# Optimization experiments

Measured on AMD Instinct MI355X. Metric: run time of the kernel, lower is better.

The kernel has to match this reference:

```python
import jax, jax.numpy as jnp
import numpy as np

T = 200                      # TRAIN_ROIS_PER_IMAGE
RATIO = 0.33                 # ROI_POSITIVE_RATIO
P_MAX = int(T * RATIO)       # max positive ROIs (66)
MH, MW = 28, 28              # MASK_SHAPE
STD = jnp.array([0.1, 0.1, 0.2, 0.2], jnp.float32)  # BBOX_STD_DEV
EPS = 1e-6


def _iou(a, b):
    # a [N,4], b [G,4] -> [N,G] IoU (same math as overlaps_graph, without tiling)
    ay1, ax1, ay2, ax2 = a[:, 0:1], a[:, 1:2], a[:, 2:3], a[:, 3:4]
    by1, bx1, by2, bx2 = b[None, :, 0], b[None, :, 1], b[None, :, 2], b[None, :, 3]
    iy = jnp.maximum(jnp.minimum(ay2, by2) - jnp.maximum(ay1, by1), 0.0)
    ix = jnp.maximum(jnp.minimum(ax2, bx2) - jnp.maximum(ax1, bx1), 0.0)
    inter = iy * ix
    union = (ay2 - ay1) * (ax2 - ax1) + (by2 - by1) * (bx2 - bx1) - inter
    return inter / jnp.maximum(union, EPS)


def _box_refinement(box, gt):
    # standard Mask R-CNN box_refinement_graph
    h = jnp.maximum(box[:, 2] - box[:, 0], EPS)
    w = jnp.maximum(box[:, 3] - box[:, 1], EPS)
    cy = box[:, 0] + 0.5 * h
    cx = box[:, 1] + 0.5 * w
    gh = jnp.maximum(gt[:, 2] - gt[:, 0], EPS)
    gw = jnp.maximum(gt[:, 3] - gt[:, 1], EPS)
    gcy = gt[:, 0] + 0.5 * gh
    gcx = gt[:, 1] + 0.5 * gw
    return jnp.stack([(gcy - cy) / h, (gcx - cx) / w,
                      jnp.log(gh / h), jnp.log(gw / w)], axis=-1)


def _crop_and_resize(imgs, boxes):
    # imgs [T,H,W], boxes [T,4] normalized; TF crop_and_resize bilinear semantics,
    # extrapolation_value = 0 for samples outside [0, H-1] x [0, W-1].
    Tn, H, W = imgs.shape
    y1, x1, y2, x2 = boxes[:, 0], boxes[:, 1], boxes[:, 2], boxes[:, 3]
    iy = jnp.arange(MH, dtype=jnp.float32)
    ix = jnp.arange(MW, dtype=jnp.float32)
    ys = y1[:, None] * (H - 1) + iy[None, :] * ((y2 - y1) * (H - 1) / (MH - 1))[:, None]  # [T,MH]
    xs = x1[:, None] * (W - 1) + ix[None, :] * ((x2 - x1) * (W - 1) / (MW - 1))[:, None]  # [T,MW]
    y0 = jnp.floor(ys); x0 = jnp.floor(xs)
    wy = (ys - y0)[:, :, None]
    wx = (xs - x0)[:, None, :]
    y0i = jnp.clip(y0, 0, H - 1).astype(jnp.int32)
    y1i = jnp.clip(y0 + 1, 0, H - 1).astype(jnp.int32)
    x0i = jnp.clip(x0, 0, W - 1).astype(jnp.int32)
    x1i = jnp.clip(x0 + 1, 0, W - 1).astype(jnp.int32)
    t = jnp.arange(Tn)[:, None, None]
    v00 = imgs[t, y0i[:, :, None], x0i[:, None, :]]
    v01 = imgs[t, y0i[:, :, None], x1i[:, None, :]]
    v10 = imgs[t, y1i[:, :, None], x0i[:, None, :]]
    v11 = imgs[t, y1i[:, :, None], x1i[:, None, :]]
    val = (v00 * (1 - wx) + v01 * wx) * (1 - wy) + (v10 * (1 - wx) + v11 * wx) * wy
    ok = ((ys >= 0) & (ys <= H - 1))[:, :, None] & ((xs >= 0) & (xs <= W - 1))[:, None, :]
    return jnp.where(ok, val, 0.0)


def _targets_one(proposals, class_ids, boxes, masks):
    # proposals [N,4], class_ids [G] int, boxes [G,4], masks [H,W,G]
    N = proposals.shape[0]
    # zero-padding trim expressed as validity masks (jit-friendly fixed shapes)
    valid_prop = jnp.any(proposals != 0, axis=1)
    valid_gt = jnp.any(boxes != 0, axis=1)
    non_crowd = (class_ids > 0) & valid_gt
    crowd = (class_ids < 0) & valid_gt

    ov = _iou(proposals, boxes)                              # [N,G]
    ov_nc = jnp.where(non_crowd[None, :], ov, -1.0)          # mask crowd/padded gt
    roi_iou_max = ov_nc.max(axis=1)
    crowd_max = jnp.where(crowd[None, :], ov, 0.0).max(axis=1)

    pos_mask = valid_prop & (roi_iou_max >= 0.5)
    neg_mask = valid_prop & (roi_iou_max < 0.5) & (crowd_max < 0.001)

    # deterministic selection (original uses tf.random.shuffle): positives first-in-order
    pos_order = jnp.argsort(jnp.where(pos_mask, 0, 1))
    neg_order = jnp.argsort(jnp.where(neg_mask, 0, 1))
    pos_count = jnp.minimum(pos_mask.sum(), P_MAX)
    neg_needed = jnp.floor(pos_count.astype(jnp.float32) / RATIO).astype(jnp.int32) - pos_count
    neg_count = jnp.minimum(jnp.minimum(neg_needed, neg_mask.sum()), T - pos_count)

    slot = jnp.arange(T)
    is_pos = slot < pos_count
    is_neg = (slot >= pos_count) & (slot < pos_count + neg_count)
    src = jnp.where(is_pos,
                    pos_order[jnp.clip(slot, 0, N - 1)],
                    neg_order[jnp.clip(slot - pos_count, 0, N - 1)])
    rois = jnp.where((is_pos | is_neg)[:, None], proposals[src], 0.0)

    assign = jnp.argmax(ov_nc[src], axis=1)                  # gt assignment per slot
    gt_box = boxes[assign]
    gt_cls = jnp.where(is_pos, class_ids[assign], 0)

    deltas = _box_refinement(rois, gt_box) / STD
    deltas = jnp.where(is_pos[:, None], deltas, 0.0)

    # USE_MINI_MASK: roi box in gt-box-normalized coordinates
    gy1, gx1, gy2, gx2 = gt_box[:, 0], gt_box[:, 1], gt_box[:, 2], gt_box[:, 3]
    gh = jnp.maximum(gy2 - gy1, EPS)
    gw = jnp.maximum(gx2 - gx1, EPS)
    mm = jnp.stack([(rois[:, 0] - gy1) / gh, (rois[:, 1] - gx1) / gw,
                    (rois[:, 2] - gy1) / gh, (rois[:, 3] - gx1) / gw], axis=-1)

    roi_masks = jnp.moveaxis(jnp.take(masks, assign, axis=2), 2, 0)  # [T,H,W]
    m = jnp.round(_crop_and_resize(roi_masks, mm))
    m = jnp.where(is_pos[:, None, None], m, 0.0)
    return rois, gt_cls, deltas, m


def setup_inputs() -> dict:
    key = jax.random.key(0)
    ks = jax.random.split(key, 4)
    B, N, G, HM = 16, 2000, 200, 56

    def boxes_of(k, shape):
        k1, k2, k3, k4 = jax.random.split(k, 4)
        y1 = jax.random.uniform(k1, shape) * 0.5
        x1 = jax.random.uniform(k2, shape) * 0.5
        h = 0.1 + jax.random.uniform(k3, shape) * 0.4
        w = 0.1 + jax.random.uniform(k4, shape) * 0.4
        return jnp.stack([y1, x1, y1 + h, x1 + w], axis=-1)

    proposals = boxes_of(ks[0], (B, N))
    proposals = proposals * (jnp.arange(N) < N - 200)[None, :, None]  # zero-padded tail
    prior_class_ids = jax.random.randint(ks[1], (B, G), -1, 81).astype(jnp.int32)  # -1=crowd, 0=padding
    prior_boxes = boxes_of(ks[2], (B, G)) * (prior_class_ids != 0)[..., None]
    prior_masks = (jax.random.uniform(ks[3], (B, HM, HM, G)) > 0.5).astype(jnp.float32)
    return {"proposals": proposals, "prior_class_ids": prior_class_ids,
            "prior_boxes": prior_boxes, "prior_masks": prior_masks}


def reference(proposals, prior_class_ids, prior_boxes, prior_masks):
    rois, cls, deltas, masks = jax.vmap(_targets_one)(proposals, prior_class_ids,
                                                      prior_boxes, prior_masks)
    return rois, cls, deltas, masks
```

## Files before the change

kernel.cpp:

```cpp
#include <hip/hip_runtime.h>
#include <math.h>

#pragma clang fp contract(off)

#define BN    16
#define NP    2000
#define NG    200
#define NT    200
#define PMAX  66
#define EPSF  1e-6f
#define MH    28
#define MW    28
#define HM    56
#define NPIX  (HM*HM)
#define NW    49
#define NGP   256

#define KA_BLOCKS 128
#define KG_BLOCKS (49*4*BN)

__global__ __launch_bounds__(256) void kF(
    const float* __restrict__ proposals, const int* __restrict__ cls_ids,
    const float* __restrict__ boxes, const float* __restrict__ masks,
    int* __restrict__ flag_ws, int* __restrict__ assign_ws,
    unsigned long long* __restrict__ bits)
{
#pragma clang fp contract(off)
  const int tid  = threadIdx.x;
  const int lane = tid & 63;
  const int wv   = tid >> 6;

  __shared__ float4 gbox[NG];
  __shared__ float  garea[NG];
  __shared__ int    gflag[NG];
  __shared__ unsigned long long sw[64];

  if (blockIdx.x < KA_BLOCKS) {
    const int b = blockIdx.x >> 3;
    const int bxa = blockIdx.x & 7;

    for (int j = tid; j < NG; j += 256) {
      float4 g = reinterpret_cast<const float4*>(boxes + (size_t)b * NG * 4)[j];
      int c = cls_ids[b * NG + j];
      bool vg = (g.x != 0.f) || (g.y != 0.f) || (g.z != 0.f) || (g.w != 0.f);
      gbox[j]  = g;
      garea[j] = (g.z - g.x) * (g.w - g.y);
      gflag[j] = vg ? (c > 0 ? 1 : (c < 0 ? 2 : 0)) : 0;
    }
    __syncthreads();

    int i = bxa * 256 + tid;
    if (i >= NP) return;

    float4 p = reinterpret_cast<const float4*>(proposals + (size_t)b * NP * 4)[i];
    bool vp = (p.x != 0.f) || (p.y != 0.f) || (p.z != 0.f) || (p.w != 0.f);
    float pa = (p.z - p.x) * (p.w - p.y);

    float best = -3.0e38f;
    int   bestj = 0;
    float cmax = 0.f;
    for (int j = 0; j < NG; ++j) {
      float4 g = gbox[j];
      float iy = fmaxf(fminf(p.z, g.z) - fmaxf(p.x, g.x), 0.f);
      float ix = fmaxf(fminf(p.w, g.w) - fmaxf(p.y, g.y), 0.f);
      float inter = iy * ix;
      float uni = (pa + garea[j]) - inter;
      float iou = inter / fmaxf(uni, EPSF);
      int fl = gflag[j];
      float v = (fl == 1) ? iou : -1.0f;
      if (v > best) { best = v; bestj = j; }
      if (fl == 2) cmax = fmaxf(cmax, iou);
    }
    bool pos = vp && (best >= 0.5f);
    bool neg = vp && (best < 0.5f) && (cmax < 0.001f);
    flag_ws[b * NP + i]   = pos ? 1 : (neg ? 2 : 0);
    assign_ws[b * NP + i] = bestj;
  } else {
    int idx = blockIdx.x - KA_BLOCKS;
    const int pword = idx % 49;
    idx /= 49;
    const int gw0 = (idx & 3) * 64;
    const int b   = idx >> 2;
    const int p0  = pword * 64;

    const bool gok = (gw0 + lane) < NG;
    const float* mbase = masks + (size_t)b * NPIX * NG + gw0 + lane;
    for (int e = 0; e < 16; ++e) {
      int pl = e * 4 + wv;
      float v = 0.f;
      if (gok) v = mbase[(size_t)(p0 + pl) * NG];
      unsigned long long word = __ballot(v != 0.f);
      if (lane == 0) sw[pl] = word;
    }
    __syncthreads();

    unsigned long long w0 = sw[lane];
    for (int k = 0; k < 16; ++k) {
      int gl = wv * 16 + k;
      unsigned long long word = __ballot((int)((w0 >> gl) & 1ULL));
      if (lane == 0 && (gw0 + gl) < NG)
        bits[(size_t)(b * NGP + gw0 + gl) * NW + pword] = word;
    }
  }
}

__global__ __launch_bounds__(256) void kB(
    const float* __restrict__ proposals, const int* __restrict__ cls_ids,
    const float* __restrict__ boxes, const int* __restrict__ flag_ws,
    const int* __restrict__ assign_ws, float* __restrict__ out,
    float* __restrict__ mm_ws, int* __restrict__ ma_ws)
{
#pragma clang fp contract(off)
  const int b = blockIdx.x;
  const int tid = threadIdx.x;
  const int lane = tid & 63;
  const int wv = tid >> 6;

  __shared__ unsigned short pos_list[NP];
  __shared__ unsigned short neg_list[NP];
  __shared__ int wcp[4], wcn[4];
  __shared__ int s_pt, s_nt;
  if (tid == 0) { s_pt = 0; s_nt = 0; }
  __syncthreads();

  const int* fb = flag_ws + b * NP;
  for (int base = 0; base < NP; base += 256) {
    int i = base + tid;
    int f = (i < NP) ? fb[i] : 0;
    bool isp = (f == 1), isn = (f == 2);
    unsigned long long bp = __ballot(isp);
    unsigned long long bn = __ballot(isn);
    __syncthreads();
    if (lane == 0) { wcp[wv] = __popcll(bp); wcn[wv] = __popcll(bn); }
    __syncthreads();
    int prep = __popcll(bp & ((1ull << lane) - 1ull));
    int pren = __popcll(bn & ((1ull << lane) - 1ull));
    int bpp = 0, bnn = 0, tp = 0, tn = 0;
    for (int w = 0; w < 4; ++w) {
      if (w < wv) { bpp += wcp[w]; bnn += wcn[w]; }
      tp += wcp[w]; tn += wcn[w];
    }
    int pt = s_pt, nt = s_nt;
    if (isp) pos_list[pt + bpp + prep] = (unsigned short)i;
    if (isn) neg_list[nt + bnn + pren] = (unsigned short)i;
    __syncthreads();
    if (tid == 0) { s_pt = pt + tp; s_nt = nt + tn; }
  }
  __syncthreads();

  int pos_total = s_pt, neg_total = s_nt;
  int pos_count = min(pos_total, PMAX);
  int neg_needed = (int)floorf((float)pos_count / 0.33f) - pos_count;
  int neg_count = min(min(neg_needed, neg_total), NT - pos_count);

  if (tid < NT) {
    bool ispos = tid < pos_count;
    bool isneg = (!ispos) && (tid < pos_count + neg_count);
    float r0 = 0.f, r1 = 0.f, r2 = 0.f, r3 = 0.f;
    float d0 = 0.f, d1 = 0.f, d2 = 0.f, d3 = 0.f;
    float m0 = 0.f, m1 = 0.f, m2 = 0.f, m3 = 0.f;
    float clsf = 0.f;
    int ma = -1;
    if (ispos || isneg) {
      int i = ispos ? (int)pos_list[tid] : (int)neg_list[tid - pos_count];
      float4 p = reinterpret_cast<const float4*>(proposals + (size_t)b * NP * 4)[i];
      r0 = p.x; r1 = p.y; r2 = p.z; r3 = p.w;
      if (ispos) {
        int a = assign_ws[b * NP + i];
        ma = a;
        float4 g = reinterpret_cast<const float4*>(boxes + (size_t)b * NG * 4)[a];
        float h  = fmaxf(r2 - r0, EPSF);
        float w  = fmaxf(r3 - r1, EPSF);
        float cy = r0 + 0.5f * h;
        float cx = r1 + 0.5f * w;
        float gh = fmaxf(g.z - g.x, EPSF);
        float gw = fmaxf(g.w - g.y, EPSF);
        float gcy = g.x + 0.5f * gh;
        float gcx = g.y + 0.5f * gw;
        d0 = ((gcy - cy) / h) / 0.1f;
        d1 = ((gcx - cx) / w) / 0.1f;
        d2 = logf(gh / h) / 0.2f;
        d3 = logf(gw / w) / 0.2f;
        m0 = (r0 - g.x) / gh;
        m1 = (r1 - g.y) / gw;
        m2 = (r2 - g.x) / gh;
        m3 = (r3 - g.y) / gw;
        clsf = (float)cls_ids[b * NG + a];
      }
    }
    int s = b * NT + tid;
    float* rois = out;
    float* cls  = out + BN * NT * 4;
    float* dlt  = out + BN * NT * 4 + BN * NT;
    rois[s * 4 + 0] = r0; rois[s * 4 + 1] = r1;
    rois[s * 4 + 2] = r2; rois[s * 4 + 3] = r3;
    cls[s] = clsf;
    dlt[s * 4 + 0] = d0; dlt[s * 4 + 1] = d1;
    dlt[s * 4 + 2] = d2; dlt[s * 4 + 3] = d3;
    mm_ws[s * 4 + 0] = m0; mm_ws[s * 4 + 1] = m1;
    mm_ws[s * 4 + 2] = m2; mm_ws[s * 4 + 3] = m3;
    ma_ws[s] = ma;
  }
}

__global__ __launch_bounds__(256) void kC(
    const unsigned long long* __restrict__ bits, const float* __restrict__ mm_ws,
    const int* __restrict__ ma_ws, float* __restrict__ out)
{
#pragma clang fp contract(off)
  const int s = blockIdx.x;
  float4* om = reinterpret_cast<float4*>(
      out + (size_t)(BN * NT * 9) + (size_t)s * (MH * MW));
  const int q = threadIdx.x;
  const int a = ma_ws[s];
  if (a < 0) {
    if (q < (MH * MW) / 4) om[q] = make_float4(0.f, 0.f, 0.f, 0.f);
    return;
  }

  __shared__ unsigned long long pb[NW];
  const int b = s / NT;
  if (q < NW) pb[q] = bits[(size_t)(b * NGP + a) * NW + q];
  __syncthreads();
  if (q >= (MH * MW) / 4) return;

  float y1 = mm_ws[s * 4 + 0], x1 = mm_ws[s * 4 + 1];
  float y2 = mm_ws[s * 4 + 2], x2 = mm_ws[s * 4 + 3];
  float sy = (y2 - y1) * 55.0f / 27.0f;
  float sx = (x2 - x1) * 55.0f / 27.0f;

  int px0 = q * 4;
  int my  = px0 / MW;
  float ys = y1 * 55.0f + (float)my * sy;
  float y0f = floorf(ys);
  float wy  = ys - y0f;
  int y0i = (int)fminf(fmaxf(y0f, 0.f), 55.f);
  int y1i = (int)fminf(fmaxf(y0f + 1.0f, 0.f), 55.f);
  bool oky = (ys >= 0.f) && (ys <= 55.f);
  const int r0b = y0i * HM;
  const int r1b = y1i * HM;

  float res[4];
  for (int k = 0; k < 4; ++k) {
    int mx = (px0 + k) - my * MW;
    float xs = x1 * 55.0f + (float)mx * sx;
    float x0f = floorf(xs);
    float wx  = xs - x0f;
    int x0i = (int)fminf(fmaxf(x0f, 0.f), 55.f);
    int x1i = (int)fminf(fmaxf(x0f + 1.0f, 0.f), 55.f);
    int p00 = r0b + x0i, p01 = r0b + x1i;
    int p10 = r1b + x0i, p11 = r1b + x1i;
    float v00 = (float)((pb[p00 >> 6] >> (p00 & 63)) & 1ULL);
    float v01 = (float)((pb[p01 >> 6] >> (p01 & 63)) & 1ULL);
    float v10 = (float)((pb[p10 >> 6] >> (p10 & 63)) & 1ULL);
    float v11 = (float)((pb[p11 >> 6] >> (p11 & 63)) & 1ULL);
    float val = (v00 * (1.f - wx) + v01 * wx) * (1.f - wy)
              + (v10 * (1.f - wx) + v11 * wx) * wy;
    bool ok = oky && (xs >= 0.f) && (xs <= 55.f);
    res[k] = ok ? rintf(val) : 0.f;
  }
  om[q] = make_float4(res[0], res[1], res[2], res[3]);
}

extern "C" void kernel_launch(void* const* d_in, const int* in_sizes, int n_in,
                              void* d_out, int out_size, void* d_ws, size_t ws_size,
                              hipStream_t stream)
{
  const float* proposals = (const float*)d_in[0];
  const int*   cls_ids   = (const int*)d_in[1];
  const float* boxes     = (const float*)d_in[2];
  const float* masks     = (const float*)d_in[3];
  float* out = (float*)d_out;

  char* ws = (char*)d_ws;
  int*   flag_ws   = (int*)ws;    ws += (size_t)BN * NP * sizeof(int);
  int*   assign_ws = (int*)ws;    ws += (size_t)BN * NP * sizeof(int);
  float* mm_ws     = (float*)ws;  ws += (size_t)BN * NT * 4 * sizeof(float);
  int*   ma_ws     = (int*)ws;    ws += (size_t)BN * NT * sizeof(int);
  unsigned long long* bits_ws = (unsigned long long*)ws;

  kF<<<KA_BLOCKS + KG_BLOCKS, 256, 0, stream>>>(
      proposals, cls_ids, boxes, masks, flag_ws, assign_ws, bits_ws);
  kB<<<BN, 256, 0, stream>>>(proposals, cls_ids, boxes, flag_ws, assign_ws,
                             out, mm_ws, ma_ws);
  kC<<<BN * NT, 256, 0, stream>>>(bits_ws, mm_ws, ma_ws, out);
}
```

Measured before the change: 112.3 us.

## Fuse ROI selection and mask crop into one kernel via ballot bitmasks

The IoU stage now writes per-wave ballot bitmasks of positive and negative proposals instead of per-proposal flags. The separate compaction kernel and mask kernel are merged into a single kernel with one block per output ROI. Each block popcounts the bitmasks to get the counts and finds its proposal with a rank-select scan, then crops the mask directly. This removes one kernel launch, the serial per-image compaction loop, and the intermediate mm/ma workspace round trip. The cost is that every block redundantly recomputes the counts and does a bit-clearing select loop that can run for up to about 64 iterations.

```diff
diff --git a/kernel.cpp b/kernel.cpp
--- a/kernel.cpp
+++ b/kernel.cpp
@@ -15,6 +15,7 @@
 #define NPIX  (HM*HM)
 #define NW    49
 #define NGP   256
+#define NPW   32
 
 #define KA_BLOCKS 128
 #define KG_BLOCKS (49*4*BN)
@@ -22,7 +23,7 @@
 __global__ __launch_bounds__(256) void kF(
     const float* __restrict__ proposals, const int* __restrict__ cls_ids,
     const float* __restrict__ boxes, const float* __restrict__ masks,
-    int* __restrict__ flag_ws, int* __restrict__ assign_ws,
+    unsigned long long* __restrict__ selbits, int* __restrict__ assign_ws,
     unsigned long long* __restrict__ bits)
 {
 #pragma clang fp contract(off)
@@ -49,11 +50,12 @@
     }
     __syncthreads();
 
-    int i = bxa * 256 + tid;
-    if (i >= NP) return;
-
-    float4 p = reinterpret_cast<const float4*>(proposals + (size_t)b * NP * 4)[i];
-    bool vp = (p.x != 0.f) || (p.y != 0.f) || (p.z != 0.f) || (p.w != 0.f);
+    const int i  = bxa * 256 + tid;
+    const bool act = (i < NP);
+    const int ic = act ? i : (NP - 1);
+
+    float4 p = reinterpret_cast<const float4*>(proposals + (size_t)b * NP * 4)[ic];
+    bool vp = act && ((p.x != 0.f) || (p.y != 0.f) || (p.z != 0.f) || (p.w != 0.f));
     float pa = (p.z - p.x) * (p.w - p.y);
 
     float best = -3.0e38f;
@@ -73,8 +75,14 @@
     }
     bool pos = vp && (best >= 0.5f);
     bool neg = vp && (best < 0.5f) && (cmax < 0.001f);
-    flag_ws[b * NP + i]   = pos ? 1 : (neg ? 2 : 0);
-    assign_ws[b * NP + i] = bestj;
+    unsigned long long bp = __ballot(pos);
+    unsigned long long bn = __ballot(neg);
+    if (lane == 0) {
+      int w = bxa * 4 + wv;
+      selbits[(size_t)b * 64 + w]       = bp;
+      selbits[(size_t)b * 64 + 32 + w]  = bn;
+    }
+    if (act) assign_ws[b * NP + i] = bestj;
   } else {
     int idx = blockIdx.x - KA_BLOCKS;
     const int pword = idx % 49;
@@ -104,91 +112,82 @@
   }
 }
 
-__global__ __launch_bounds__(256) void kB(
+__global__ __launch_bounds__(256) void kS(
     const float* __restrict__ proposals, const int* __restrict__ cls_ids,
-    const float* __restrict__ boxes, const int* __restrict__ flag_ws,
-    const int* __restrict__ assign_ws, float* __restrict__ out,
-    float* __restrict__ mm_ws, int* __restrict__ ma_ws)
+    const float* __restrict__ boxes, const int* __restrict__ assign_ws,
+    const unsigned long long* __restrict__ selbits,
+    const unsigned long long* __restrict__ bits, float* __restrict__ out)
 {
 #pragma clang fp contract(off)
-  const int b = blockIdx.x;
-  const int tid = threadIdx.x;
-  const int lane = tid & 63;
-  const int wv = tid >> 6;
-
-  __shared__ unsigned short pos_list[NP];
-  __shared__ unsigned short neg_list[NP];
-  __shared__ int wcp[4], wcn[4];
-  __shared__ int s_pt, s_nt;
-  if (tid == 0) { s_pt = 0; s_nt = 0; }
+  const int s = blockIdx.x;
+  const int b = s / NT;
+  const int t = s - b * NT;
+  const int q = threadIdx.x;
+
+  __shared__ unsigned long long sel[64];
+  __shared__ unsigned long long pb[NW];
+
+  if (q < 64) sel[q] = selbits[(size_t)b * 64 + q];
   __syncthreads();
 
-  const int* fb = flag_ws + b * NP;
-  for (int base = 0; base < NP; base += 256) {
-    int i = base + tid;
-    int f = (i < NP) ? fb[i] : 0;
-    bool isp = (f == 1), isn = (f == 2);
-    unsigned long long bp = __ballot(isp);
-    unsigned long long bn = __ballot(isn);
-    __syncthreads();
-    if (lane == 0) { wcp[wv] = __popcll(bp); wcn[wv] = __popcll(bn); }
-    __syncthreads();
-    int prep = __popcll(bp & ((1ull << lane) - 1ull));
-    int pren = __popcll(bn & ((1ull << lane) - 1ull));
-    int bpp = 0, bnn = 0, tp = 0, tn = 0;
-    for (int w = 0; w < 4; ++w) {
-      if (w < wv) { bpp += wcp[w]; bnn += wcn[w]; }
-      tp += wcp[w]; tn += wcn[w];
-    }
-    int pt = s_pt, nt = s_nt;
-    if (isp) pos_list[pt + bpp + prep] = (unsigned short)i;
-    if (isn) neg_list[nt + bnn + pren] = (unsigned short)i;
-    __syncthreads();
-    if (tid == 0) { s_pt = pt + tp; s_nt = nt + tn; }
-  }
-  __syncthreads();
-
-  int pos_total = s_pt, neg_total = s_nt;
+  int pos_total = 0, neg_total = 0;
+  for (int w = 0; w < NPW; ++w) {
+    pos_total += __popcll(sel[w]);
+    neg_total += __popcll(sel[32 + w]);
+  }
   int pos_count = min(pos_total, PMAX);
   int neg_needed = (int)floorf((float)pos_count / 0.33f) - pos_count;
   int neg_count = min(min(neg_needed, neg_total), NT - pos_count);
 
-  if (tid < NT) {
-    bool ispos = tid < pos_count;
-    bool isneg = (!ispos) && (tid < pos_count + neg_count);
-    float r0 = 0.f, r1 = 0.f, r2 = 0.f, r3 = 0.f;
-    float d0 = 0.f, d1 = 0.f, d2 = 0.f, d3 = 0.f;
-    float m0 = 0.f, m1 = 0.f, m2 = 0.f, m3 = 0.f;
-    float clsf = 0.f;
-    int ma = -1;
-    if (ispos || isneg) {
-      int i = ispos ? (int)pos_list[tid] : (int)neg_list[tid - pos_count];
-      float4 p = reinterpret_cast<const float4*>(proposals + (size_t)b * NP * 4)[i];
-      r0 = p.x; r1 = p.y; r2 = p.z; r3 = p.w;
-      if (ispos) {
-        int a = assign_ws[b * NP + i];
-        ma = a;
-        float4 g = reinterpret_cast<const float4*>(boxes + (size_t)b * NG * 4)[a];
-        float h  = fmaxf(r2 - r0, EPSF);
-        float w  = fmaxf(r3 - r1, EPSF);
-        float cy = r0 + 0.5f * h;
-        float cx = r1 + 0.5f * w;
-        float gh = fmaxf(g.z - g.x, EPSF);
-        float gw = fmaxf(g.w - g.y, EPSF);
-        float gcy = g.x + 0.5f * gh;
-        float gcx = g.y + 0.5f * gw;
-        d0 = ((gcy - cy) / h) / 0.1f;
-        d1 = ((gcx - cx) / w) / 0.1f;
-        d2 = logf(gh / h) / 0.2f;
-        d3 = logf(gw / w) / 0.2f;
-        m0 = (r0 - g.x) / gh;
-        m1 = (r1 - g.y) / gw;
-        m2 = (r2 - g.x) / gh;
-        m3 = (r3 - g.y) / gw;
-        clsf = (float)cls_ids[b * NG + a];
+  const bool ispos = (t < pos_count);
+  const bool isneg = (!ispos) && (t < pos_count + neg_count);
+
+  float r0 = 0.f, r1 = 0.f, r2 = 0.f, r3 = 0.f;
+  float d0 = 0.f, d1 = 0.f, d2 = 0.f, d3 = 0.f;
+  float m0 = 0.f, m1 = 0.f, m2 = 0.f, m3 = 0.f;
+  float clsf = 0.f;
+  int a = -1;
+
+  if (ispos || isneg) {
+    int k = ispos ? t : (t - pos_count);
+    const int base = ispos ? 0 : 32;
+    int i = 0;
+    for (int w = 0; w < NPW; ++w) {
+      unsigned long long word = sel[base + w];
+      int c = __popcll(word);
+      if (k < c) {
+        for (int r = 0; r < k; ++r) word &= word - 1ULL;
+        i = w * 64 + __builtin_ctzll(word);
+        break;
       }
-    }
-    int s = b * NT + tid;
+      k -= c;
+    }
+    float4 p = reinterpret_cast<const float4*>(proposals + (size_t)b * NP * 4)[i];
+    r0 = p.x; r1 = p.y; r2 = p.z; r3 = p.w;
+    if (ispos) {
+      a = assign_ws[b * NP + i];
+      float4 g = reinterpret_cast<const float4*>(boxes + (size_t)b * NG * 4)[a];
+      float h  = fmaxf(r2 - r0, EPSF);
+      float w  = fmaxf(r3 - r1, EPSF);
+      float cy = r0 + 0.5f * h;
+      float cx = r1 + 0.5f * w;
+      float gh = fmaxf(g.z - g.x, EPSF);
+      float gw = fmaxf(g.w - g.y, EPSF);
+      float gcy = g.x + 0.5f * gh;
+      float gcx = g.y + 0.5f * gw;
+      d0 = ((gcy - cy) / h) / 0.1f;
+      d1 = ((gcx - cx) / w) / 0.1f;
+      d2 = logf(gh / h) / 0.2f;
+      d3 = logf(gw / w) / 0.2f;
+      m0 = (r0 - g.x) / gh;
+      m1 = (r1 - g.y) / gw;
+      m2 = (r2 - g.x) / gh;
+      m3 = (r3 - g.y) / gw;
+      clsf = (float)cls_ids[b * NG + a];
+    }
+  }
+
+  if (q == 0) {
     float* rois = out;
     float* cls  = out + BN * NT * 4;
     float* dlt  = out + BN * NT * 4 + BN * NT;
@@ -197,41 +196,25 @@
     cls[s] = clsf;
     dlt[s * 4 + 0] = d0; dlt[s * 4 + 1] = d1;
     dlt[s * 4 + 2] = d2; dlt[s * 4 + 3] = d3;
-    mm_ws[s * 4 + 0] = m0; mm_ws[s * 4 + 1] = m1;
-    mm_ws[s * 4 + 2] = m2; mm_ws[s * 4 + 3] = m3;
-    ma_ws[s] = ma;
-  }
-}
-
-__global__ __launch_bounds__(256) void kC(
-    const unsigned long long* __restrict__ bits, const float* __restrict__ mm_ws,
-    const int* __restrict__ ma_ws, float* __restrict__ out)
-{
-#pragma clang fp contract(off)
-  const int s = blockIdx.x;
+  }
+
   float4* om = reinterpret_cast<float4*>(
       out + (size_t)(BN * NT * 9) + (size_t)s * (MH * MW));
-  const int q = threadIdx.x;
-  const int a = ma_ws[s];
-  if (a < 0) {
+  if (!ispos) {
     if (q < (MH * MW) / 4) om[q] = make_float4(0.f, 0.f, 0.f, 0.f);
     return;
   }
 
-  __shared__ unsigned long long pb[NW];
-  const int b = s / NT;
   if (q < NW) pb[q] = bits[(size_t)(b * NGP + a) * NW + q];
   __syncthreads();
   if (q >= (MH * MW) / 4) return;
 
-  float y1 = mm_ws[s * 4 + 0], x1 = mm_ws[s * 4 + 1];
-  float y2 = mm_ws[s * 4 + 2], x2 = mm_ws[s * 4 + 3];
-  float sy = (y2 - y1) * 55.0f / 27.0f;
-  float sx = (x2 - x1) * 55.0f / 27.0f;
+  float sy = (m2 - m0) * 55.0f / 27.0f;
+  float sx = (m3 - m1) * 55.0f / 27.0f;
 
   int px0 = q * 4;
   int my  = px0 / MW;
-  float ys = y1 * 55.0f + (float)my * sy;
+  float ys = m0 * 55.0f + (float)my * sy;
   float y0f = floorf(ys);
   float wy  = ys - y0f;
   int y0i = (int)fminf(fmaxf(y0f, 0.f), 55.f);
@@ -243,7 +226,7 @@
   float res[4];
   for (int k = 0; k < 4; ++k) {
     int mx = (px0 + k) - my * MW;
-    float xs = x1 * 55.0f + (float)mx * sx;
+    float xs = m1 * 55.0f + (float)mx * sx;
     float x0f = floorf(xs);
     float wx  = xs - x0f;
     int x0i = (int)fminf(fmaxf(x0f, 0.f), 55.f);
@@ -273,15 +256,14 @@
   float* out = (float*)d_out;
 
   char* ws = (char*)d_ws;
-  int*   flag_ws   = (int*)ws;    ws += (size_t)BN * NP * sizeof(int);
-  int*   assign_ws = (int*)ws;    ws += (size_t)BN * NP * sizeof(int);
-  float* mm_ws     = (float*)ws;  ws += (size_t)BN * NT * 4 * sizeof(float);
-  int*   ma_ws     = (int*)ws;    ws += (size_t)BN * NT * sizeof(int);
+  unsigned long long* selbits = (unsigned long long*)ws;
+  ws += (size_t)BN * 64 * sizeof(unsigned long long);
   unsigned long long* bits_ws = (unsigned long long*)ws;
+  ws += (size_t)BN * NGP * NW * sizeof(unsigned long long);
+  int* assign_ws = (int*)ws;
 
   kF<<<KA_BLOCKS + KG_BLOCKS, 256, 0, stream>>>(
-      proposals, cls_ids, boxes, masks, flag_ws, assign_ws, bits_ws);
-  kB<<<BN, 256, 0, stream>>>(proposals, cls_ids, boxes, flag_ws, assign_ws,
-                             out, mm_ws, ma_ws);
-  kC<<<BN * NT, 256, 0, stream>>>(bits_ws, mm_ws, ma_ws, out);
+      proposals, cls_ids, boxes, masks, selbits, assign_ws, bits_ws);
+  kS<<<BN * NT, 256, 0, stream>>>(proposals, cls_ids, boxes, assign_ws,
+                                  selbits, bits_ws, out);
 }
```

Result: slower. 116.0 us (+3.3%).
